# Kernel tuning notes

Measured on AMD Instinct MI355X. Metric: run time of the kernel, lower is better.

Reference implementation:

```python
import jax, jax.numpy as jnp
import numpy as np

SCALE = 1.0  # scale argument passed to titans_memory_forward in the original forward


def setup_inputs() -> dict:
    key = jax.random.key(0)
    k1, k2, k3 = jax.random.split(key, 3)
    B, N, D = 4096, 32768, 1024
    x = jax.random.normal(k1, (B, D), dtype=jnp.float32)
    memory_keys = jax.random.normal(k2, (N, D), dtype=jnp.float32)
    memory_values = jax.random.normal(k3, (N, D), dtype=jnp.float32)
    return {"x": x, "memory_keys": memory_keys, "memory_values": memory_values}


def reference(x, memory_keys, memory_values):
    # Associative memory retrieval: similarity scores -> softmax -> weighted sum of values.
    # scores: [B, N]
    scores = jnp.einsum('bd,nd->bn', x, memory_keys) * SCALE
    attn = jax.nn.softmax(scores, axis=-1)
    # output: [B, D]
    out = jnp.einsum('bn,nd->bd', attn, memory_values)
    return out
```

## Files before the change

kernel.cpp:

```cpp
#include <hip/hip_runtime.h>

typedef _Float16 f16;
typedef _Float16 f16x8 __attribute__((ext_vector_type(8)));
typedef float f32x4 __attribute__((ext_vector_type(4)));

#define B_ 4096
#define N_ 32768
#define D_ 1024
#define BM 32
#define BN 256
#define COLS 32
#define THREADS 512
#define DSLICE 128
#define NHALF (N_ / 2)
#define ITERS (NHALF / BN)

__device__ __forceinline__ f32x4 mfma16(f16x8 a, f16x8 b, f32x4 c) {
    return __builtin_amdgcn_mfma_f32_16x16x32_f16(a, b, c, 0, 0, 0);
}

__global__ void conv_kf(const float* __restrict__ K, f16* __restrict__ Kf) {
    int tid = blockIdx.x * 256 + threadIdx.x;
    int g = tid >> 6, lane = tid & 63;
    int rb = g >> 5, ks = g & 31;
    int l15 = lane & 15, lg = lane >> 4;
    const float* s = K + (size_t)(rb * 16 + l15) * D_ + ks * 32 + lg * 8;
    float4 a = *(const float4*)s, b = *(const float4*)(s + 4);
    f16x8 h;
    h[0] = (f16)a.x; h[1] = (f16)a.y; h[2] = (f16)a.z; h[3] = (f16)a.w;
    h[4] = (f16)b.x; h[5] = (f16)b.y; h[6] = (f16)b.z; h[7] = (f16)b.w;
    *(f16x8*)(Kf + (size_t)tid * 8) = h;
}

__global__ void conv_vf(const float* __restrict__ V, f16* __restrict__ Vf) {
    int tid = blockIdx.x * 256 + threadIdx.x;
    int g = tid >> 6, lane = tid & 63;
    int db = g & 63, kb = g >> 6;
    int l15 = lane & 15, lg = lane >> 4;
    const float* s = V + (size_t)(kb * 32 + lg * 8) * D_ + db * 16 + l15;
    f16x8 h;
    #pragma unroll
    for (int j = 0; j < 8; ++j) h[j] = (f16)s[(size_t)j * D_];
    *(f16x8*)(Vf + (size_t)tid * 8) = h;
}

__global__ __launch_bounds__(THREADS, 2)
void attn_main(const float* __restrict__ Xg, const f16* __restrict__ Kf,
               const f16* __restrict__ Vf, float* __restrict__ Opart,
               float* __restrict__ Mpart, float* __restrict__ Lpart)
{
    __shared__ __align__(16) f16 Xh[BM * D_];
    __shared__ __align__(16) f16 Pl[BM * BN];
    __shared__ float2 red[BM][9];

    const int xcd   = blockIdx.x & 7;
    const int chunk = xcd >> 2;
    const int bblk  = ((blockIdx.x >> 3) << 2) | (xcd & 3);
    const int kvbase = chunk * NHALF;
    const int b0 = bblk * BM;
    const int t  = threadIdx.x;

    for (int c = t; c < BM * D_ / 8; c += THREADS) {
        int dblk = c >> 7;
        int row  = (c >> 2) & 31;
        int sub  = c & 3;
        int d0   = dblk * 32 + sub * 8;
        const float* s = Xg + (size_t)(b0 + row) * D_ + d0;
        float4 a = *(const float4*)s, b = *(const float4*)(s + 4);
        f16x8 hi;
        hi[0] = (f16)a.x; hi[1] = (f16)a.y; hi[2] = (f16)a.z; hi[3] = (f16)a.w;
        hi[4] = (f16)b.x; hi[5] = (f16)b.y; hi[6] = (f16)b.z; hi[7] = (f16)b.w;
        *(f16x8*)((char*)Xh + dblk * 2048 + row * 64 + sub * 16) = hi;
    }
    __syncthreads();

    const int wave = t >> 6, lane = t & 63;
    const int l15 = lane & 15, lg = lane >> 4;
    const int cw = wave * COLS;

    const char* bh0 = (const char*)Xh + l15 * 64 + lg * 16;
    const char* bh1 = (const char*)Xh + (l15 + 16) * 64 + lg * 16;
    const char* pr0 = (const char*)Pl + l15 * 64 + lg * 16;
    const char* pr1 = (const char*)Pl + (l15 + 16) * 64 + lg * 16;

    const f16* kp0 = Kf + ((size_t)(kvbase / 16 + wave * 2) * 32 * 64 + lane) * 8;
    const f16* kp1 = kp0 + 16384;
    const f16* vbase = Vf + (((size_t)(kvbase / 32) * 64 + wave * 8) * 64 + lane) * 8;

    f32x4 S[2][2];
    f16x8 kA[8], kB[8];

    auto LOADK = [&](f16x8* buf, int ks0) {
        #pragma unroll
        for (int j = 0; j < 4; ++j) {
            buf[2 * j]     = *(const f16x8*)(kp0 + (ks0 + j) * 512);
            buf[2 * j + 1] = *(const f16x8*)(kp1 + (ks0 + j) * 512);
        }
    };
    auto USEK = [&](const f16x8* kb2, int ks0) {
        #pragma unroll
        for (int j = 0; j < 4; ++j) {
            int ks = ks0 + j;
            f16x8 ah0 = *(const f16x8*)(bh0 + ks * 2048);
            f16x8 ah1 = *(const f16x8*)(bh1 + ks * 2048);
            __builtin_amdgcn_s_setprio(1);
            S[0][0] = mfma16(ah0, kb2[2 * j],     S[0][0]);
            S[0][1] = mfma16(ah0, kb2[2 * j + 1], S[0][1]);
            S[1][0] = mfma16(ah1, kb2[2 * j],     S[1][0]);
            S[1][1] = mfma16(ah1, kb2[2 * j + 1], S[1][1]);
            __builtin_amdgcn_s_setprio(0);
        }
    };
    auto QK = [&]() {
        #pragma unroll
        for (int rg = 0; rg < 2; ++rg)
            #pragma unroll
            for (int cg = 0; cg < 2; ++cg) S[rg][cg] = (f32x4){0.f, 0.f, 0.f, 0.f};
        LOADK(kA, 0);
        LOADK(kB, 4);  USEK(kA, 0);
        LOADK(kA, 8);  USEK(kB, 4);
        LOADK(kB, 12); USEK(kA, 8);
        LOADK(kA, 16); USEK(kB, 12);
        LOADK(kB, 20); USEK(kA, 16);
        LOADK(kA, 24); USEK(kB, 20);
        LOADK(kB, 28); USEK(kA, 24);
                       USEK(kB, 28);
    };

    f32x4 O[2][8];
    #pragma unroll
    for (int rg = 0; rg < 2; ++rg)
        #pragma unroll
        for (int fn = 0; fn < 8; ++fn) O[rg][fn] = (f32x4){0.f, 0.f, 0.f, 0.f};
    float mq[8];
    #pragma unroll
    for (int u = 0; u < 8; ++u) mq[u] = -INFINITY;
    float m2a = -INFINITY, m2b = -INFINITY, l2a = 0.f, l2b = 0.f;

    f16x8 vA[8], vB[8];
    auto LOADV = [&](f16x8* buf, int ks2) {
        #pragma unroll
        for (int fn = 0; fn < 8; ++fn)
            buf[fn] = *(const f16x8*)(vbase + ks2 * 32768 + fn * 512);
    };
    float ba[8], bb[8];
    auto USEV = [&](const f16x8* vb2, int ks2) {
        f16 ba16 = (f16)ba[ks2], bb16 = (f16)bb[ks2];
        f16x8 pa0 = *(const f16x8*)(pr0 + ks2 * 2048);
        f16x8 pa1 = *(const f16x8*)(pr1 + ks2 * 2048);
        #pragma unroll
        for (int j = 0; j < 8; ++j) { pa0[j] *= ba16; pa1[j] *= bb16; }
        __builtin_amdgcn_s_setprio(1);
        #pragma unroll
        for (int fn = 0; fn < 8; ++fn) {
            O[0][fn] = mfma16(pa0, vb2[fn], O[0][fn]);
            O[1][fn] = mfma16(pa1, vb2[fn], O[1][fn]);
        }
        __builtin_amdgcn_s_setprio(0);
    };

    QK();

    for (int it = 0; it < ITERS; ++it) {
        #pragma unroll
        for (int rg = 0; rg < 2; ++rg)
            #pragma unroll
            for (int i = 0; i < 4; ++i) {
                float a = S[rg][0][i], b = S[rg][1][i];
                float mx = fmaxf(a, b);
                mx = fmaxf(mx, __shfl_xor(mx, 1));
                mx = fmaxf(mx, __shfl_xor(mx, 2));
                mx = fmaxf(mx, __shfl_xor(mx, 4));
                mx = fmaxf(mx, __shfl_xor(mx, 8));
                float p0 = __expf(a - mx), p1 = __expf(b - mx);
                float s = p0 + p1;
                s += __shfl_xor(s, 1);
                s += __shfl_xor(s, 2);
                s += __shfl_xor(s, 4);
                s += __shfl_xor(s, 8);
                int m = rg * 16 + lg * 4 + i;
                int off0 = wave * 2048 + m * 64 + ((l15 >> 3) << 4) + ((l15 & 7) << 1);
                *(f16*)((char*)Pl + off0)      = (f16)p0;
                *(f16*)((char*)Pl + off0 + 32) = (f16)p1;
                if (l15 == 0) red[m][wave] = make_float2(mx, s);
            }
        __syncthreads();

        LOADV(vA, 0);
        LOADV(vB, 1);

        float M2an = m2a, M2bn = m2b;
        #pragma unroll
        for (int s2 = 0; s2 < 8; ++s2) {
            M2an = fmaxf(M2an, red[l15][s2].x);
            M2bn = fmaxf(M2bn, red[l15 + 16][s2].x);
        }
        float laa = 0.f, lbb = 0.f;
        #pragma unroll
        for (int s2 = 0; s2 < 8; ++s2) {
            float2 ra = red[l15][s2], rb = red[l15 + 16][s2];
            ba[s2] = __expf(ra.x - M2an); laa += ra.y * ba[s2];
            bb[s2] = __expf(rb.x - M2bn); lbb += rb.y * bb[s2];
        }
        l2a = l2a * __expf(m2a - M2an) + laa; m2a = M2an;
        l2b = l2b * __expf(m2b - M2bn) + lbb; m2b = M2bn;

        float al[2][4];
        #pragma unroll
        for (int rg = 0; rg < 2; ++rg)
            #pragma unroll
            for (int i = 0; i < 4; ++i) {
                int u = rg * 4 + i;
                int src = (lane & 48) | (lg * 4 + i);
                float Mq = __shfl(rg ? M2bn : M2an, src);
                al[rg][i] = __expf(mq[u] - Mq);
                mq[u] = Mq;
            }
        #pragma unroll
        for (int rg = 0; rg < 2; ++rg)
            #pragma unroll
            for (int fn = 0; fn < 8; ++fn)
                #pragma unroll
                for (int i = 0; i < 4; ++i)
                    O[rg][fn][i] *= al[rg][i];

        USEV(vA, 0);  LOADV(vA, 2);
        USEV(vB, 1);  LOADV(vB, 3);
        USEV(vA, 2);  LOADV(vA, 4);
        USEV(vB, 3);  LOADV(vB, 5);
        USEV(vA, 4);  LOADV(vA, 6);
        USEV(vB, 5);  LOADV(vB, 7);
        USEV(vA, 6);
        USEV(vB, 7);

        kp0 += (size_t)16 * 16384;
        kp1 += (size_t)16 * 16384;
        vbase += (size_t)8 * 32768;
        if (it + 1 < ITERS) QK();
        __syncthreads();
    }

    float* Op = Opart + (size_t)chunk * B_ * D_;
    #pragma unroll
    for (int rg = 0; rg < 2; ++rg)
        #pragma unroll
        for (int fn = 0; fn < 8; ++fn)
            #pragma unroll
            for (int i = 0; i < 4; ++i) {
                int row = b0 + rg * 16 + lg * 4 + i;
                int col = wave * DSLICE + fn * 16 + l15;
                Op[(size_t)row * D_ + col] = O[rg][fn][i];
            }
    if (wave == 0 && lg == 0) {
        Mpart[(size_t)chunk * B_ + b0 + l15]      = m2a;
        Lpart[(size_t)chunk * B_ + b0 + l15]      = l2a;
        Mpart[(size_t)chunk * B_ + b0 + 16 + l15] = m2b;
        Lpart[(size_t)chunk * B_ + b0 + 16 + l15] = l2b;
    }
}

__global__ void combine_k(const float* __restrict__ Opart,
                          const float* __restrict__ Mp, const float* __restrict__ Lp,
                          float* __restrict__ Outg)
{
    int b = blockIdx.x;
    float m0 = Mp[b], m1 = Mp[B_ + b];
    float l0 = Lp[b], l1 = Lp[B_ + b];
    float M  = fmaxf(m0, m1);
    float w0 = __expf(m0 - M), w1 = __expf(m1 - M);
    float inv = 1.f / (w0 * l0 + w1 * l1);
    const float4* O0 = (const float4*)(Opart + (size_t)b * D_);
    const float4* O1 = (const float4*)(Opart + (size_t)B_ * D_ + (size_t)b * D_);
    float4* o = (float4*)(Outg + (size_t)b * D_);
    for (int i = threadIdx.x; i < D_ / 4; i += blockDim.x) {
        float4 a = O0[i], c = O1[i];
        float4 r;
        r.x = (w0 * a.x + w1 * c.x) * inv;
        r.y = (w0 * a.y + w1 * c.y) * inv;
        r.z = (w0 * a.z + w1 * c.z) * inv;
        r.w = (w0 * a.w + w1 * c.w) * inv;
        o[i] = r;
    }
}

extern "C" void kernel_launch(void* const* d_in, const int* in_sizes, int n_in,
                              void* d_out, int out_size, void* d_ws, size_t ws_size,
                              hipStream_t stream) {
    const float* X = (const float*)d_in[0];
    const float* K = (const float*)d_in[1];
    const float* V = (const float*)d_in[2];
    float* Out = (float*)d_out;

    const size_t szKf = (size_t)N_ * D_ * sizeof(f16);
    const size_t szVf = (size_t)N_ * D_ * sizeof(f16);
    const size_t szOp = 2ull * B_ * D_ * sizeof(float);
    const size_t szM  = 2ull * B_ * sizeof(float);

    f16*   Kf = (f16*)d_ws;
    f16*   Vf = (f16*)((char*)d_ws + szKf);
    float* Op = (float*)((char*)d_ws + szKf + szVf);
    float* Mp = (float*)((char*)Op + szOp);
    float* Lp = (float*)((char*)Mp + szM);

    conv_kf<<<(N_ * D_ / 8) / 256, 256, 0, stream>>>(K, Kf);
    conv_vf<<<(N_ * D_ / 8) / 256, 256, 0, stream>>>(V, Vf);
    attn_main<<<256, THREADS, 0, stream>>>(X, Kf, Vf, Op, Mp, Lp);
    combine_k<<<B_, 256, 0, stream>>>(Op, Mp, Lp, Out);
}
```

Measured before the change: 884.3 us.

## Double-buffer P tile and reductions to drop barrier; skip unneeded O rescale

Makes the LDS probability tile and the per-wave max/sum reduction array double-buffered by iteration parity, which lets the trailing __syncthreads at the end of each loop iteration go away. Each iteration now needs one block barrier instead of two. It also skips the O accumulator rescale when no row max grew in the wave, using a wave-wide __any vote. The cost is doubled shared memory for Pl and red, which may hurt occupancy at two blocks per CU. Correctness relies on one barrier per iteration being enough to keep the ping-pong buffers apart.

```diff
diff --git a/kernel.cpp b/kernel.cpp
--- a/kernel.cpp
+++ b/kernel.cpp
@@ -9,7 +9,6 @@
 #define D_ 1024
 #define BM 32
 #define BN 256
-#define COLS 32
 #define THREADS 512
 #define DSLICE 128
 #define NHALF (N_ / 2)
@@ -50,8 +49,8 @@
                float* __restrict__ Mpart, float* __restrict__ Lpart)
 {
     __shared__ __align__(16) f16 Xh[BM * D_];
-    __shared__ __align__(16) f16 Pl[BM * BN];
-    __shared__ float2 red[BM][9];
+    __shared__ __align__(16) f16 Pl[2][BM * BN];
+    __shared__ float2 red[2][BM][9];
 
     const int xcd   = blockIdx.x & 7;
     const int chunk = xcd >> 2;
@@ -76,12 +75,11 @@
 
     const int wave = t >> 6, lane = t & 63;
     const int l15 = lane & 15, lg = lane >> 4;
-    const int cw = wave * COLS;
 
     const char* bh0 = (const char*)Xh + l15 * 64 + lg * 16;
     const char* bh1 = (const char*)Xh + (l15 + 16) * 64 + lg * 16;
-    const char* pr0 = (const char*)Pl + l15 * 64 + lg * 16;
-    const char* pr1 = (const char*)Pl + (l15 + 16) * 64 + lg * 16;
+    const char* pr0 = (const char*)&Pl[0][0] + l15 * 64 + lg * 16;
+    const char* pr1 = (const char*)&Pl[0][0] + (l15 + 16) * 64 + lg * 16;
 
     const f16* kp0 = Kf + ((size_t)(kvbase / 16 + wave * 2) * 32 * 64 + lane) * 8;
     const f16* kp1 = kp0 + 16384;
@@ -89,6 +87,7 @@
 
     f32x4 S[2][2];
     f16x8 kA[8], kB[8];
+    int pbOfs = 0;
 
     auto LOADK = [&](f16x8* buf, int ks0) {
         #pragma unroll
@@ -146,8 +145,8 @@
     float ba[8], bb[8];
     auto USEV = [&](const f16x8* vb2, int ks2) {
         f16 ba16 = (f16)ba[ks2], bb16 = (f16)bb[ks2];
-        f16x8 pa0 = *(const f16x8*)(pr0 + ks2 * 2048);
-        f16x8 pa1 = *(const f16x8*)(pr1 + ks2 * 2048);
+        f16x8 pa0 = *(const f16x8*)(pr0 + pbOfs + ks2 * 2048);
+        f16x8 pa1 = *(const f16x8*)(pr1 + pbOfs + ks2 * 2048);
         #pragma unroll
         for (int j = 0; j < 8; ++j) { pa0[j] *= ba16; pa1[j] *= bb16; }
         __builtin_amdgcn_s_setprio(1);
@@ -160,6 +159,7 @@
     };
 
     QK();
+    int pb = 0;
 
     for (int it = 0; it < ITERS; ++it) {
         #pragma unroll
@@ -179,50 +179,56 @@
                 s += __shfl_xor(s, 4);
                 s += __shfl_xor(s, 8);
                 int m = rg * 16 + lg * 4 + i;
-                int off0 = wave * 2048 + m * 64 + ((l15 >> 3) << 4) + ((l15 & 7) << 1);
-                *(f16*)((char*)Pl + off0)      = (f16)p0;
-                *(f16*)((char*)Pl + off0 + 32) = (f16)p1;
-                if (l15 == 0) red[m][wave] = make_float2(mx, s);
+                int off0 = pb * 16384 + wave * 2048 + m * 64
+                         + ((l15 >> 3) << 4) + ((l15 & 7) << 1);
+                *(f16*)((char*)&Pl[0][0] + off0)      = (f16)p0;
+                *(f16*)((char*)&Pl[0][0] + off0 + 32) = (f16)p1;
+                if (l15 == 0) red[pb][m][wave] = make_float2(mx, s);
             }
         __syncthreads();
 
+        pbOfs = pb * 16384;
+
         LOADV(vA, 0);
         LOADV(vB, 1);
 
+        float m2a0 = m2a, m2b0 = m2b;
         float M2an = m2a, M2bn = m2b;
         #pragma unroll
         for (int s2 = 0; s2 < 8; ++s2) {
-            M2an = fmaxf(M2an, red[l15][s2].x);
-            M2bn = fmaxf(M2bn, red[l15 + 16][s2].x);
+            M2an = fmaxf(M2an, red[pb][l15][s2].x);
+            M2bn = fmaxf(M2bn, red[pb][l15 + 16][s2].x);
         }
         float laa = 0.f, lbb = 0.f;
         #pragma unroll
         for (int s2 = 0; s2 < 8; ++s2) {
-            float2 ra = red[l15][s2], rb = red[l15 + 16][s2];
+            float2 ra = red[pb][l15][s2], rb = red[pb][l15 + 16][s2];
             ba[s2] = __expf(ra.x - M2an); laa += ra.y * ba[s2];
             bb[s2] = __expf(rb.x - M2bn); lbb += rb.y * bb[s2];
         }
         l2a = l2a * __expf(m2a - M2an) + laa; m2a = M2an;
         l2b = l2b * __expf(m2b - M2bn) + lbb; m2b = M2bn;
 
-        float al[2][4];
-        #pragma unroll
-        for (int rg = 0; rg < 2; ++rg)
-            #pragma unroll
-            for (int i = 0; i < 4; ++i) {
-                int u = rg * 4 + i;
-                int src = (lane & 48) | (lg * 4 + i);
-                float Mq = __shfl(rg ? M2bn : M2an, src);
-                al[rg][i] = __expf(mq[u] - Mq);
-                mq[u] = Mq;
-            }
-        #pragma unroll
-        for (int rg = 0; rg < 2; ++rg)
-            #pragma unroll
-            for (int fn = 0; fn < 8; ++fn)
+        if (__any((M2an > m2a0) || (M2bn > m2b0))) {
+            float al[2][4];
+            #pragma unroll
+            for (int rg = 0; rg < 2; ++rg)
                 #pragma unroll
-                for (int i = 0; i < 4; ++i)
-                    O[rg][fn][i] *= al[rg][i];
+                for (int i = 0; i < 4; ++i) {
+                    int u = rg * 4 + i;
+                    int src = (lane & 48) | (lg * 4 + i);
+                    float Mq = __shfl(rg ? M2bn : M2an, src);
+                    al[rg][i] = __expf(mq[u] - Mq);
+                    mq[u] = Mq;
+                }
+            #pragma unroll
+            for (int rg = 0; rg < 2; ++rg)
+                #pragma unroll
+                for (int fn = 0; fn < 8; ++fn)
+                    #pragma unroll
+                    for (int i = 0; i < 4; ++i)
+                        O[rg][fn][i] *= al[rg][i];
+        }
 
         USEV(vA, 0);  LOADV(vA, 2);
         USEV(vB, 1);  LOADV(vB, 3);
@@ -237,7 +243,7 @@
         kp1 += (size_t)16 * 16384;
         vbase += (size_t)8 * 32768;
         if (it + 1 < ITERS) QK();
-        __syncthreads();
+        pb ^= 1;
     }
 
     float* Op = Opart + (size_t)chunk * B_ * D_;
```

New measurement: 876.3 us, median of 3. About the same (-0.9%).
